# Kernel optimization log

Measured on AMD Instinct MI355X. Metric: run time of the kernel, lower is better.

The kernel has to match this reference:

```python
import jax, jax.numpy as jnp
import numpy as np

CAP = 512  # per-expert capacity; mean tokens/expert = 4096*4/64 = 256, CAP = mean + ~16 sigma (no drops for seed 0)


def _moe_forward(hidden_states, gate_w, w13, w2, top_k):
    T, H = hidden_states.shape
    E = gate_w.shape[0]
    # --- gating: softmax over expert logits, then top-k (npu_moe_gating_top_k_softmax) ---
    logits = hidden_states @ gate_w.T                      # [T, E]
    probs = jax.nn.softmax(logits, axis=-1)
    topk_w, topk_idx = jax.lax.top_k(probs, top_k)         # [T, K]
    # norm_topk_prob=True and top_k > 1
    topk_w = topk_w / (topk_w.sum(axis=-1, keepdims=True) + 1e-20)
    # --- init_routing: compute each (token, slot)'s rank within its expert ---
    N = T * top_k
    flat_e = topk_idx.reshape(N)                           # [N] expert id per expanded row
    order = jnp.argsort(flat_e)                            # stable sort by expert
    sorted_e = flat_e[order]
    counts = jax.ops.segment_sum(jnp.ones((N,), jnp.int32), flat_e, num_segments=E)
    starts = jnp.cumsum(counts) - counts                   # [E] start offset of each expert group
    rank_sorted = jnp.arange(N, dtype=jnp.int32) - starts[sorted_e].astype(jnp.int32)
    rank = jnp.zeros((N,), jnp.int32).at[order].set(rank_sorted)  # within-expert position
    # --- dispatch into [E, CAP, H] buffers (token gather/scatter) ---
    x_rep = jnp.repeat(hidden_states, top_k, axis=0)       # [N, H]
    disp = jnp.zeros((E, CAP, H), hidden_states.dtype).at[flat_e, rank].set(x_rep)
    # --- grouped GEMM: SwiGLU expert FFN as batched matmuls ---
    h = jnp.einsum('ech,ehf->ecf', disp, w13)              # [E, CAP, 2I]
    g, u = jnp.split(h, 2, axis=-1)
    a = jax.nn.silu(g) * u                                 # [E, CAP, I]
    y = jnp.einsum('eci,eih->ech', a, w2)                  # [E, CAP, H]
    # --- finalize_routing: gather back and weighted combine ---
    out_rows = y[flat_e, rank]                             # [N, H]
    out = (out_rows.reshape(T, top_k, H) * topk_w[..., None]).sum(axis=1)
    return out


def setup_inputs() -> dict:
    key = jax.random.key(0)
    k1, k2, k3, k4 = jax.random.split(key, 4)
    T, H, E, I = 4096, 2048, 64, 768
    hidden_states = jax.random.normal(k1, (T, H), dtype=jnp.float32)
    gate_w = jax.random.normal(k2, (E, H), dtype=jnp.float32) * 0.02
    w13 = jax.random.normal(k3, (E, H, 2 * I), dtype=jnp.float32) * 0.02
    w2 = jax.random.normal(k4, (E, I, H), dtype=jnp.float32) * 0.02
    return {"hidden_states": hidden_states, "gate_w": gate_w, "w13": w13, "w2": w2, "top_k": 4}


def reference(hidden_states, gate_w, w13, w2, top_k):
    return _moe_forward(hidden_states, gate_w, w13, w2, top_k)
```

## Files before the change

### kernel.cpp

```cpp
#include <hip/hip_runtime.h>
#include <hip/hip_bf16.h>

#define T_TOK 4096
#define HDIM  2048
#define NEXP  64
#define IDIM  768
#define TOPK  4
#define CAPE  512
#define NFLAT (T_TOK*TOPK)

typedef __bf16        bf16x8 __attribute__((ext_vector_type(8)));
typedef float         f32x4  __attribute__((ext_vector_type(4)));
typedef unsigned int  u32x4  __attribute__((ext_vector_type(4)));

__device__ __forceinline__ unsigned short f2bf(float f) {
  __bf16 b = (__bf16)f;
  return __builtin_bit_cast(unsigned short, b);
}
__device__ __forceinline__ unsigned pack2(float lo, float hi) {
  return (unsigned)f2bf(lo) | ((unsigned)f2bf(hi) << 16);
}

__global__ __launch_bounds__(256) void k_gating(
    const float* __restrict__ hs, const float* __restrict__ gw,
    unsigned short* __restrict__ hs_bf, int* __restrict__ tidx, float* __restrict__ tw)
{
  __shared__ float lg[16][64];
  const int tid = threadIdx.x;
  const int t0  = blockIdx.x * 16;

  {
    const f32x4* src = (const f32x4*)(hs + (size_t)t0 * HDIM);
    for (int i = tid; i < 16 * HDIM / 4; i += 256) {
      f32x4 v = src[i];
      ushort4 o;
      o.x = f2bf(v[0]); o.y = f2bf(v[1]); o.z = f2bf(v[2]); o.w = f2bf(v[3]);
      *(ushort4*)(hs_bf + (size_t)t0 * HDIM + (size_t)i * 4) = o;
    }
  }

  const int lane = tid & 63, wv = tid >> 6;
  {
    const f32x4* gr = (const f32x4*)(gw + (size_t)lane * HDIM);
    const f32x4* x0 = (const f32x4*)(hs + (size_t)(t0 + wv*4 + 0) * HDIM);
    const f32x4* x1 = (const f32x4*)(hs + (size_t)(t0 + wv*4 + 1) * HDIM);
    const f32x4* x2 = (const f32x4*)(hs + (size_t)(t0 + wv*4 + 2) * HDIM);
    const f32x4* x3 = (const f32x4*)(hs + (size_t)(t0 + wv*4 + 3) * HDIM);
    float a0=0.f, a1=0.f, a2=0.f, a3=0.f;
    for (int h = 0; h < HDIM/4; ++h) {
      f32x4 g = gr[h];
      f32x4 v0 = x0[h], v1 = x1[h], v2 = x2[h], v3 = x3[h];
      a0 += g[0]*v0[0] + g[1]*v0[1] + g[2]*v0[2] + g[3]*v0[3];
      a1 += g[0]*v1[0] + g[1]*v1[1] + g[2]*v1[2] + g[3]*v1[3];
      a2 += g[0]*v2[0] + g[1]*v2[1] + g[2]*v2[2] + g[3]*v2[3];
      a3 += g[0]*v3[0] + g[1]*v3[1] + g[2]*v3[2] + g[3]*v3[3];
    }
    lg[wv*4+0][lane] = a0;
    lg[wv*4+1][lane] = a1;
    lg[wv*4+2][lane] = a2;
    lg[wv*4+3][lane] = a3;
  }
  __syncthreads();

  if (tid < 16) {
    const int t = t0 + tid;
    unsigned long long chosen = 0ull;
    float bv[4]; int bi[4];
#pragma unroll
    for (int k = 0; k < 4; ++k) {
      float best = -1e30f; int b = 0;
      for (int e = 0; e < 64; ++e) {
        float v = lg[tid][e];
        if (!((chosen >> e) & 1ull) && v > best) { best = v; b = e; }
      }
      chosen |= 1ull << b; bv[k] = best; bi[k] = b;
    }
    float s = 0.f, w[4];
#pragma unroll
    for (int k = 0; k < 4; ++k) { w[k] = __expf(bv[k] - bv[0]); s += w[k]; }
    float inv = 1.f / s;
#pragma unroll
    for (int k = 0; k < 4; ++k) { tidx[t*4+k] = bi[k]; tw[t*4+k] = w[k] * inv; }
  }
}

__global__ __launch_bounds__(64) void k_count_rank(
    const int* __restrict__ tidx, int* __restrict__ rankb, int* __restrict__ counts)
{
  const int e = blockIdx.x;
  const int lane = threadIdx.x;
  int base = 0;
  for (int c = 0; c < NFLAT/64; ++c) {
    int n = c*64 + lane;
    bool m = (tidx[n] == e);
    unsigned long long mask = __ballot(m);
    if (m) rankb[n] = base + __popcll(mask & ((1ull << lane) - 1ull));
    base += __popcll(mask);
  }
  if (lane == 0) counts[e] = base;
}

__global__ __launch_bounds__(256) void k_build(
    const int* __restrict__ tidx, const int* __restrict__ rankb,
    const int* __restrict__ counts,
    int* __restrict__ starts, int* __restrict__ row_info, int* __restrict__ sortpos)
{
  __shared__ int s_starts[NEXP];
  if (threadIdx.x == 0) {
    int s = 0;
    for (int e = 0; e < NEXP; ++e) { s_starts[e] = s; starts[e] = s; s += counts[e]; }
  }
  __syncthreads();
  for (int n = threadIdx.x; n < NFLAT; n += 256) {
    int e = tidx[n], r = rankb[n];
    int sr = s_starts[e] + r;
    row_info[sr] = n;
    sortpos[n] = (r < CAPE) ? sr : -1;
  }
}

__global__ __launch_bounds__(512, 2) void k_gemm1(
    const unsigned short* __restrict__ hs_bf, const float* __restrict__ w13,
    const int* __restrict__ counts, const int* __restrict__ starts,
    const int* __restrict__ row_info, unsigned short* __restrict__ a_buf)
{
  const int nt = blockIdx.x;
  const int mt = blockIdx.y;
  const int e  = blockIdx.z;
  const int count = min(counts[e], CAPE);
  const int R0 = mt * 256;
  if (R0 >= count) return;
  const int tid = threadIdx.x;
  const int base_sorted = starts[e] + R0;

  __shared__ __align__(16) char lds[2*32768];
  char* Alds = lds;
  char* Bgl  = lds + 32768;
  char* Bul  = lds + 32768 + 16384;

  const int mrow = tid >> 3, cchunk = tid & 7;
  int tokp[4];
#pragma unroll
  for (int p = 0; p < 4; ++p) {
    int sr = base_sorted + mrow + p*64;
    if (sr > NFLAT-1) sr = NFLAT-1;
    tokp[p] = row_info[sr] >> 2;
  }
  const float* w13e = w13 + (size_t)e * HDIM * (2*IDIM);
  const int half = tid >> 8;
  const int t8   = tid & 255;
  const int kg   = t8 >> 5;
  const int n4   = (t8 & 31) * 4;

  const int lane = tid & 63, wv = tid >> 6;
  const int wr = wv >> 1, wc = wv & 1;

  f32x4 accg[4][4], accu[4][4];
#pragma unroll
  for (int i = 0; i < 4; ++i)
#pragma unroll
    for (int j = 0; j < 4; ++j) { accg[i][j] = f32x4{0.f,0.f,0.f,0.f}; accu[i][j] = f32x4{0.f,0.f,0.f,0.f}; }

  for (int kt = 0; kt < HDIM/64; ++kt) {
#pragma unroll
    for (int p = 0; p < 4; ++p) {
      int m = mrow + p*64;
      u32x4 v = *(const u32x4*)(hs_bf + (size_t)tokp[p]*HDIM + kt*64 + cchunk*8);
      *(u32x4*)(Alds + m*128 + ((cchunk ^ (m & 7)) << 4)) = v;
    }
    {
      const float* bp = w13e + (size_t)(kt*64 + kg*8) * (2*IDIM) + half*IDIM + nt*128 + n4;
      f32x4 f[8];
#pragma unroll
      for (int j = 0; j < 8; ++j) f[j] = *(const f32x4*)(bp + (size_t)j * (2*IDIM));
      char* Bl = half ? Bul : Bgl;
#pragma unroll
      for (int i = 0; i < 4; ++i) {
        int n = n4 + i;
        u32x4 q;
        q[0] = pack2(f[0][i], f[1][i]);
        q[1] = pack2(f[2][i], f[3][i]);
        q[2] = pack2(f[4][i], f[5][i]);
        q[3] = pack2(f[6][i], f[7][i]);
        *(u32x4*)(Bl + n*128 + ((kg ^ (n & 7)) << 4)) = q;
      }
    }
    __syncthreads();
#pragma unroll
    for (int kfi = 0; kfi < 2; ++kfi) {
      bf16x8 af[4], bg[4], bu[4];
#pragma unroll
      for (int mi = 0; mi < 4; ++mi) {
        int row = wr*64 + mi*16 + (lane & 15);
        af[mi] = *(const bf16x8*)(Alds + row*128 + ((((kfi<<2)|(lane>>4)) ^ (row & 7)) << 4));
      }
#pragma unroll
      for (int ni = 0; ni < 4; ++ni) {
        int n = wc*64 + ni*16 + (lane & 15);
        int c = (((kfi<<2)|(lane>>4)) ^ (n & 7)) << 4;
        bg[ni] = *(const bf16x8*)(Bgl + n*128 + c);
        bu[ni] = *(const bf16x8*)(Bul + n*128 + c);
      }
#pragma unroll
      for (int mi = 0; mi < 4; ++mi)
#pragma unroll
        for (int ni = 0; ni < 4; ++ni) {
          accg[mi][ni] = __builtin_amdgcn_mfma_f32_16x16x32_bf16(af[mi], bg[ni], accg[mi][ni], 0, 0, 0);
          accu[mi][ni] = __builtin_amdgcn_mfma_f32_16x16x32_bf16(af[mi], bu[ni], accu[mi][ni], 0, 0, 0);
        }
    }
    __syncthreads();
  }

#pragma unroll
  for (int mi = 0; mi < 4; ++mi) {
#pragma unroll
    for (int j = 0; j < 4; ++j) {
      int rl = wr*64 + mi*16 + (lane >> 4)*4 + j;
      if (R0 + rl < count) {
        size_t rowoff = (size_t)(base_sorted + rl) * IDIM;
#pragma unroll
        for (int ni = 0; ni < 4; ++ni) {
          int col = nt*128 + wc*64 + ni*16 + (lane & 15);
          float g = accg[mi][ni][j], u = accu[mi][ni][j];
          float a = (g / (1.f + __expf(-g))) * u;
          a_buf[rowoff + col] = f2bf(a);
        }
      }
    }
  }
}

__global__ __launch_bounds__(512, 2) void k_gemm2(
    const unsigned short* __restrict__ a_buf, const float* __restrict__ w2,
    const int* __restrict__ counts, const int* __restrict__ starts,
    float* __restrict__ y_buf)
{
  const int nt = blockIdx.x;
  const int mt = blockIdx.y;
  const int e  = blockIdx.z;
  const int count = min(counts[e], CAPE);
  const int R0 = mt * 256;
  if (R0 >= count) return;
  const int tid = threadIdx.x;
  const int base_sorted = starts[e] + R0;

  __shared__ __align__(16) char lds[32768 + 32768];
  char* Alds = lds;
  char* Blds = lds + 32768;

  const int mrow = tid >> 3, cchunk = tid & 7;
  int srp[4];
#pragma unroll
  for (int p = 0; p < 4; ++p) {
    int sr = base_sorted + mrow + p*64;
    srp[p] = (sr > NFLAT-1) ? (NFLAT-1) : sr;
  }
  const float* w2e = w2 + (size_t)e * IDIM * HDIM;
  const int pass = tid >> 8;
  const int t8   = tid & 255;
  const int kg   = t8 >> 5, n4 = (t8 & 31) * 4;
  const int lane = tid & 63, wv = tid >> 6, wr = wv >> 1, wc = wv & 1;

  f32x4 acc[4][8];
#pragma unroll
  for (int i = 0; i < 4; ++i)
#pragma unroll
    for (int j = 0; j < 8; ++j) acc[i][j] = f32x4{0.f,0.f,0.f,0.f};

  for (int kt = 0; kt < IDIM/64; ++kt) {
#pragma unroll
    for (int p = 0; p < 4; ++p) {
      int m = mrow + p*64;
      u32x4 v = *(const u32x4*)(a_buf + (size_t)srp[p]*IDIM + kt*64 + cchunk*8);
      *(u32x4*)(Alds + m*128 + ((cchunk ^ (m & 7)) << 4)) = v;
    }
    {
      int nn = n4 + pass*128;
      const float* bp = w2e + (size_t)(kt*64 + kg*8) * HDIM + nt*256 + nn;
      f32x4 f[8];
#pragma unroll
      for (int j = 0; j < 8; ++j) f[j] = *(const f32x4*)(bp + (size_t)j * HDIM);
#pragma unroll
      for (int i = 0; i < 4; ++i) {
        int n = nn + i;
        u32x4 q;
        q[0] = pack2(f[0][i], f[1][i]);
        q[1] = pack2(f[2][i], f[3][i]);
        q[2] = pack2(f[4][i], f[5][i]);
        q[3] = pack2(f[6][i], f[7][i]);
        *(u32x4*)(Blds + n*128 + ((kg ^ (n & 7)) << 4)) = q;
      }
    }
    __syncthreads();
#pragma unroll
    for (int kfi = 0; kfi < 2; ++kfi) {
      bf16x8 af[4], bb[8];
#pragma unroll
      for (int mi = 0; mi < 4; ++mi) {
        int row = wr*64 + mi*16 + (lane & 15);
        af[mi] = *(const bf16x8*)(Alds + row*128 + ((((kfi<<2)|(lane>>4)) ^ (row & 7)) << 4));
      }
#pragma unroll
      for (int ni = 0; ni < 8; ++ni) {
        int n = wc*128 + ni*16 + (lane & 15);
        bb[ni] = *(const bf16x8*)(Blds + n*128 + (((((kfi<<2)|(lane>>4)) ^ (n & 7))) << 4));
      }
#pragma unroll
      for (int mi = 0; mi < 4; ++mi)
#pragma unroll
        for (int ni = 0; ni < 8; ++ni)
          acc[mi][ni] = __builtin_amdgcn_mfma_f32_16x16x32_bf16(af[mi], bb[ni], acc[mi][ni], 0, 0, 0);
    }
    __syncthreads();
  }

#pragma unroll
  for (int mi = 0; mi < 4; ++mi) {
#pragma unroll
    for (int j = 0; j < 4; ++j) {
      int rl = wr*64 + mi*16 + (lane >> 4)*4 + j;
      if (R0 + rl < count) {
        int sr = base_sorted + rl;
        float* yrow = y_buf + (size_t)sr * HDIM;
#pragma unroll
        for (int ni = 0; ni < 8; ++ni) {
          int col = nt*256 + wc*128 + ni*16 + (lane & 15);
          yrow[col] = acc[mi][ni][j];
        }
      }
    }
  }
}

__global__ __launch_bounds__(256) void k_finalize(
    const float* __restrict__ y_buf, const int* __restrict__ sortpos,
    const float* __restrict__ tw, float* __restrict__ out)
{
  const int t = blockIdx.x;
  const int tid = threadIdx.x;
  f32x4 acc0 = {0.f,0.f,0.f,0.f}, acc1 = {0.f,0.f,0.f,0.f};
#pragma unroll
  for (int k = 0; k < 4; ++k) {
    int sp = sortpos[t*4+k];
    float w = tw[t*4+k];
    if (sp >= 0) {
      const f32x4* yr = (const f32x4*)(y_buf + (size_t)sp * HDIM);
      acc0 += w * yr[tid];
      acc1 += w * yr[tid + 256];
    }
  }
  f32x4* o = (f32x4*)(out + (size_t)t * HDIM);
  o[tid] = acc0;
  o[tid + 256] = acc1;
}

extern "C" void kernel_launch(void* const* d_in, const int* in_sizes, int n_in,
                              void* d_out, int out_size, void* d_ws, size_t ws_size,
                              hipStream_t stream) {
  const float* hs  = (const float*)d_in[0];
  const float* gw  = (const float*)d_in[1];
  const float* w13 = (const float*)d_in[2];
  const float* w2  = (const float*)d_in[3];
  float* out = (float*)d_out;

  char* ws = (char*)d_ws;
  size_t off = 0;
  auto alloc = [&](size_t bytes) {
    off = (off + 255) & ~(size_t)255;
    char* p = ws + off;
    off += bytes;
    return p;
  };
  unsigned short* hs_bf = (unsigned short*)alloc((size_t)T_TOK * HDIM * 2);
  int*   tidx   = (int*)  alloc((size_t)NFLAT * 4);
  float* tw     = (float*)alloc((size_t)NFLAT * 4);
  int*   rankb  = (int*)  alloc((size_t)NFLAT * 4);
  int*   counts = (int*)  alloc((size_t)NEXP * 4);
  int*   starts = (int*)  alloc((size_t)NEXP * 4);
  int*   rinfo  = (int*)  alloc((size_t)NFLAT * 4);
  int*   sortp  = (int*)  alloc((size_t)NFLAT * 4);
  unsigned short* a_buf = (unsigned short*)alloc((size_t)NFLAT * IDIM * 2);
  float* y_buf  = (float*)alloc((size_t)NFLAT * HDIM * 4);
  (void)ws_size; (void)in_sizes; (void)n_in; (void)out_size;

  k_gating<<<T_TOK/16, 256, 0, stream>>>(hs, gw, hs_bf, tidx, tw);
  k_count_rank<<<NEXP, 64, 0, stream>>>(tidx, rankb, counts);
  k_build<<<1, 256, 0, stream>>>(tidx, rankb, counts, starts, rinfo, sortp);
  k_gemm1<<<dim3(6, 2, NEXP), 512, 0, stream>>>(hs_bf, w13, counts, starts, rinfo, a_buf);
  k_gemm2<<<dim3(8, 2, NEXP), 512, 0, stream>>>(a_buf, w2, counts, starts, y_buf);
  k_finalize<<<T_TOK, 256, 0, stream>>>(y_buf, sortp, tw, out);
}
```

Before: 796.7 us.

## Double-buffer LDS with register prefetch, loop M tiles in-block, store y as bf16

Both expert GEMMs now double-buffer LDS (128KB) and prefetch the next K tile's A rows and fp32 weights into registers while MFMAs run on the current tile, dropping one barrier per iteration. The M-tile grid dimension is folded into an in-block loop, so each block walks all of its expert's row tiles. The LDS swizzle also XORs in row>>3 bits. The intermediate y buffer is stored as bf16 instead of fp32, halving its write and read traffic in finalize at some precision cost. The larger LDS footprint likely lowers occupancy, and fewer blocks now launch (384/512 versus up to double before), which reduces parallelism.

```diff
diff --git a/kernel.cpp b/kernel.cpp
--- a/kernel.cpp
+++ b/kernel.cpp
@@ -19,6 +19,9 @@
 }
 __device__ __forceinline__ unsigned pack2(float lo, float hi) {
   return (unsigned)f2bf(lo) | ((unsigned)f2bf(hi) << 16);
+}
+__device__ __forceinline__ int swz(int row, int chunk) {
+  return row*128 + (((chunk ^ (row & 7) ^ ((row >> 3) & 7)) & 7) << 4);
 }
 
 __global__ __launch_bounds__(256) void k_gating(
@@ -125,106 +128,138 @@
     const int* __restrict__ row_info, unsigned short* __restrict__ a_buf)
 {
   const int nt = blockIdx.x;
-  const int mt = blockIdx.y;
-  const int e  = blockIdx.z;
+  const int e  = blockIdx.y;
   const int count = min(counts[e], CAPE);
-  const int R0 = mt * 256;
-  if (R0 >= count) return;
+  if (count <= 0) return;
+  const int nmt = (count + 255) >> 8;
   const int tid = threadIdx.x;
-  const int base_sorted = starts[e] + R0;
-
-  __shared__ __align__(16) char lds[2*32768];
-  char* Alds = lds;
-  char* Bgl  = lds + 32768;
-  char* Bul  = lds + 32768 + 16384;
+  const int estart = starts[e];
+
+  __shared__ __align__(16) char lds[2*65536];
 
   const int mrow = tid >> 3, cchunk = tid & 7;
-  int tokp[4];
-#pragma unroll
-  for (int p = 0; p < 4; ++p) {
-    int sr = base_sorted + mrow + p*64;
-    if (sr > NFLAT-1) sr = NFLAT-1;
-    tokp[p] = row_info[sr] >> 2;
-  }
   const float* w13e = w13 + (size_t)e * HDIM * (2*IDIM);
   const int half = tid >> 8;
   const int t8   = tid & 255;
   const int kg   = t8 >> 5;
   const int n4   = (t8 & 31) * 4;
-
   const int lane = tid & 63, wv = tid >> 6;
   const int wr = wv >> 1, wc = wv & 1;
 
-  f32x4 accg[4][4], accu[4][4];
-#pragma unroll
-  for (int i = 0; i < 4; ++i)
-#pragma unroll
-    for (int j = 0; j < 4; ++j) { accg[i][j] = f32x4{0.f,0.f,0.f,0.f}; accu[i][j] = f32x4{0.f,0.f,0.f,0.f}; }
-
-  for (int kt = 0; kt < HDIM/64; ++kt) {
+  int cur = 0;
+  for (int mi = 0; mi < nmt; ++mi) {
+    const int R0 = mi << 8;
+    const int base_sorted = estart + R0;
+    int tokp[4];
 #pragma unroll
     for (int p = 0; p < 4; ++p) {
-      int m = mrow + p*64;
-      u32x4 v = *(const u32x4*)(hs_bf + (size_t)tokp[p]*HDIM + kt*64 + cchunk*8);
-      *(u32x4*)(Alds + m*128 + ((cchunk ^ (m & 7)) << 4)) = v;
-    }
+      int sr = base_sorted + mrow + p*64;
+      if (sr > NFLAT-1) sr = NFLAT-1;
+      tokp[p] = row_info[sr] >> 2;
+    }
+    f32x4 accg[4][4], accu[4][4];
+#pragma unroll
+    for (int i = 0; i < 4; ++i)
+#pragma unroll
+      for (int j = 0; j < 4; ++j) { accg[i][j] = f32x4{0.f,0.f,0.f,0.f}; accu[i][j] = f32x4{0.f,0.f,0.f,0.f}; }
+
+    u32x4 rA[4]; f32x4 rB[8];
+#pragma unroll
+    for (int p = 0; p < 4; ++p)
+      rA[p] = *(const u32x4*)(hs_bf + (size_t)tokp[p]*HDIM + cchunk*8);
     {
-      const float* bp = w13e + (size_t)(kt*64 + kg*8) * (2*IDIM) + half*IDIM + nt*128 + n4;
-      f32x4 f[8];
-#pragma unroll
-      for (int j = 0; j < 8; ++j) f[j] = *(const f32x4*)(bp + (size_t)j * (2*IDIM));
-      char* Bl = half ? Bul : Bgl;
+      const float* bp = w13e + (size_t)(kg*8) * (2*IDIM) + half*IDIM + nt*128 + n4;
+#pragma unroll
+      for (int j = 0; j < 8; ++j) rB[j] = *(const f32x4*)(bp + (size_t)j * (2*IDIM));
+    }
+    __syncthreads();
+    {
+      char* A0 = lds + cur*65536;
+      char* B0 = lds + cur*65536 + 32768 + half*16384;
+#pragma unroll
+      for (int p = 0; p < 4; ++p)
+        *(u32x4*)(A0 + swz(mrow + p*64, cchunk)) = rA[p];
 #pragma unroll
       for (int i = 0; i < 4; ++i) {
-        int n = n4 + i;
         u32x4 q;
-        q[0] = pack2(f[0][i], f[1][i]);
-        q[1] = pack2(f[2][i], f[3][i]);
-        q[2] = pack2(f[4][i], f[5][i]);
-        q[3] = pack2(f[6][i], f[7][i]);
-        *(u32x4*)(Bl + n*128 + ((kg ^ (n & 7)) << 4)) = q;
-      }
-    }
-    __syncthreads();
-#pragma unroll
-    for (int kfi = 0; kfi < 2; ++kfi) {
-      bf16x8 af[4], bg[4], bu[4];
-#pragma unroll
-      for (int mi = 0; mi < 4; ++mi) {
-        int row = wr*64 + mi*16 + (lane & 15);
-        af[mi] = *(const bf16x8*)(Alds + row*128 + ((((kfi<<2)|(lane>>4)) ^ (row & 7)) << 4));
-      }
-#pragma unroll
-      for (int ni = 0; ni < 4; ++ni) {
-        int n = wc*64 + ni*16 + (lane & 15);
-        int c = (((kfi<<2)|(lane>>4)) ^ (n & 7)) << 4;
-        bg[ni] = *(const bf16x8*)(Bgl + n*128 + c);
-        bu[ni] = *(const bf16x8*)(Bul + n*128 + c);
-      }
-#pragma unroll
-      for (int mi = 0; mi < 4; ++mi)
+        q[0] = pack2(rB[0][i], rB[1][i]);
+        q[1] = pack2(rB[2][i], rB[3][i]);
+        q[2] = pack2(rB[4][i], rB[5][i]);
+        q[3] = pack2(rB[6][i], rB[7][i]);
+        *(u32x4*)(B0 + swz(n4 + i, kg)) = q;
+      }
+    }
+
+    for (int kt = 0; kt < HDIM/64; ++kt) {
+      __syncthreads();
+      const bool pf = (kt+1 < HDIM/64);
+      if (pf) {
+#pragma unroll
+        for (int p = 0; p < 4; ++p)
+          rA[p] = *(const u32x4*)(hs_bf + (size_t)tokp[p]*HDIM + (kt+1)*64 + cchunk*8);
+        const float* bp = w13e + (size_t)((kt+1)*64 + kg*8) * (2*IDIM) + half*IDIM + nt*128 + n4;
+#pragma unroll
+        for (int j = 0; j < 8; ++j) rB[j] = *(const f32x4*)(bp + (size_t)j * (2*IDIM));
+      }
+      char* Ac  = lds + cur*65536;
+      char* Bgc = lds + cur*65536 + 32768;
+      char* Buc = Bgc + 16384;
+#pragma unroll
+      for (int kfi = 0; kfi < 2; ++kfi) {
+        const int ch = (kfi<<2) | (lane>>4);
+        bf16x8 af[4], bg[4], bu[4];
+#pragma unroll
+        for (int mi2 = 0; mi2 < 4; ++mi2) {
+          int row = wr*64 + mi2*16 + (lane & 15);
+          af[mi2] = *(const bf16x8*)(Ac + swz(row, ch));
+        }
 #pragma unroll
         for (int ni = 0; ni < 4; ++ni) {
-          accg[mi][ni] = __builtin_amdgcn_mfma_f32_16x16x32_bf16(af[mi], bg[ni], accg[mi][ni], 0, 0, 0);
-          accu[mi][ni] = __builtin_amdgcn_mfma_f32_16x16x32_bf16(af[mi], bu[ni], accu[mi][ni], 0, 0, 0);
-        }
-    }
-    __syncthreads();
-  }
-
-#pragma unroll
-  for (int mi = 0; mi < 4; ++mi) {
-#pragma unroll
-    for (int j = 0; j < 4; ++j) {
-      int rl = wr*64 + mi*16 + (lane >> 4)*4 + j;
-      if (R0 + rl < count) {
-        size_t rowoff = (size_t)(base_sorted + rl) * IDIM;
-#pragma unroll
-        for (int ni = 0; ni < 4; ++ni) {
-          int col = nt*128 + wc*64 + ni*16 + (lane & 15);
-          float g = accg[mi][ni][j], u = accu[mi][ni][j];
-          float a = (g / (1.f + __expf(-g))) * u;
-          a_buf[rowoff + col] = f2bf(a);
+          int n = wc*64 + ni*16 + (lane & 15);
+          bg[ni] = *(const bf16x8*)(Bgc + swz(n, ch));
+          bu[ni] = *(const bf16x8*)(Buc + swz(n, ch));
+        }
+#pragma unroll
+        for (int mi2 = 0; mi2 < 4; ++mi2)
+#pragma unroll
+          for (int ni = 0; ni < 4; ++ni) {
+            accg[mi2][ni] = __builtin_amdgcn_mfma_f32_16x16x32_bf16(af[mi2], bg[ni], accg[mi2][ni], 0, 0, 0);
+            accu[mi2][ni] = __builtin_amdgcn_mfma_f32_16x16x32_bf16(af[mi2], bu[ni], accu[mi2][ni], 0, 0, 0);
+          }
+      }
+      if (pf) {
+        char* An = lds + (cur^1)*65536;
+        char* Bn = lds + (cur^1)*65536 + 32768 + half*16384;
+#pragma unroll
+        for (int p = 0; p < 4; ++p)
+          *(u32x4*)(An + swz(mrow + p*64, cchunk)) = rA[p];
+#pragma unroll
+        for (int i = 0; i < 4; ++i) {
+          u32x4 q;
+          q[0] = pack2(rB[0][i], rB[1][i]);
+          q[1] = pack2(rB[2][i], rB[3][i]);
+          q[2] = pack2(rB[4][i], rB[5][i]);
+          q[3] = pack2(rB[6][i], rB[7][i]);
+          *(u32x4*)(Bn + swz(n4 + i, kg)) = q;
+        }
+      }
+      cur ^= 1;
+    }
+
+#pragma unroll
+    for (int mi2 = 0; mi2 < 4; ++mi2) {
+#pragma unroll
+      for (int j = 0; j < 4; ++j) {
+        int rl = wr*64 + mi2*16 + (lane >> 4)*4 + j;
+        if (R0 + rl < count) {
+          size_t rowoff = (size_t)(base_sorted + rl) * IDIM;
+#pragma unroll
+          for (int ni = 0; ni < 4; ++ni) {
+            int col = nt*128 + wc*64 + ni*16 + (lane & 15);
+            float g = accg[mi2][ni][j], u = accu[mi2][ni][j];
+            float a = (g / (1.f + __expf(-g))) * u;
+            a_buf[rowoff + col] = f2bf(a);
+          }
         }
       }
     }
@@ -234,99 +269,135 @@
 __global__ __launch_bounds__(512, 2) void k_gemm2(
     const unsigned short* __restrict__ a_buf, const float* __restrict__ w2,
     const int* __restrict__ counts, const int* __restrict__ starts,
-    float* __restrict__ y_buf)
+    unsigned short* __restrict__ y_buf)
 {
   const int nt = blockIdx.x;
-  const int mt = blockIdx.y;
-  const int e  = blockIdx.z;
+  const int e  = blockIdx.y;
   const int count = min(counts[e], CAPE);
-  const int R0 = mt * 256;
-  if (R0 >= count) return;
+  if (count <= 0) return;
+  const int nmt = (count + 255) >> 8;
   const int tid = threadIdx.x;
-  const int base_sorted = starts[e] + R0;
-
-  __shared__ __align__(16) char lds[32768 + 32768];
-  char* Alds = lds;
-  char* Blds = lds + 32768;
+  const int estart = starts[e];
+
+  __shared__ __align__(16) char lds[2*65536];
 
   const int mrow = tid >> 3, cchunk = tid & 7;
-  int srp[4];
-#pragma unroll
-  for (int p = 0; p < 4; ++p) {
-    int sr = base_sorted + mrow + p*64;
-    srp[p] = (sr > NFLAT-1) ? (NFLAT-1) : sr;
-  }
   const float* w2e = w2 + (size_t)e * IDIM * HDIM;
   const int pass = tid >> 8;
   const int t8   = tid & 255;
   const int kg   = t8 >> 5, n4 = (t8 & 31) * 4;
   const int lane = tid & 63, wv = tid >> 6, wr = wv >> 1, wc = wv & 1;
 
-  f32x4 acc[4][8];
-#pragma unroll
-  for (int i = 0; i < 4; ++i)
-#pragma unroll
-    for (int j = 0; j < 8; ++j) acc[i][j] = f32x4{0.f,0.f,0.f,0.f};
-
-  for (int kt = 0; kt < IDIM/64; ++kt) {
+  int cur = 0;
+  for (int mi = 0; mi < nmt; ++mi) {
+    const int R0 = mi << 8;
+    const int base_sorted = estart + R0;
+    int srp[4];
 #pragma unroll
     for (int p = 0; p < 4; ++p) {
-      int m = mrow + p*64;
-      u32x4 v = *(const u32x4*)(a_buf + (size_t)srp[p]*IDIM + kt*64 + cchunk*8);
-      *(u32x4*)(Alds + m*128 + ((cchunk ^ (m & 7)) << 4)) = v;
-    }
+      int sr = base_sorted + mrow + p*64;
+      srp[p] = (sr > NFLAT-1) ? (NFLAT-1) : sr;
+    }
+    f32x4 acc[4][8];
+#pragma unroll
+    for (int i = 0; i < 4; ++i)
+#pragma unroll
+      for (int j = 0; j < 8; ++j) acc[i][j] = f32x4{0.f,0.f,0.f,0.f};
+
+    u32x4 rA[4]; f32x4 rB[8];
+#pragma unroll
+    for (int p = 0; p < 4; ++p)
+      rA[p] = *(const u32x4*)(a_buf + (size_t)srp[p]*IDIM + cchunk*8);
     {
-      int nn = n4 + pass*128;
-      const float* bp = w2e + (size_t)(kt*64 + kg*8) * HDIM + nt*256 + nn;
-      f32x4 f[8];
-#pragma unroll
-      for (int j = 0; j < 8; ++j) f[j] = *(const f32x4*)(bp + (size_t)j * HDIM);
+      const float* bp = w2e + (size_t)(kg*8) * HDIM + nt*256 + pass*128 + n4;
+#pragma unroll
+      for (int j = 0; j < 8; ++j) rB[j] = *(const f32x4*)(bp + (size_t)j * HDIM);
+    }
+    __syncthreads();
+    {
+      char* A0 = lds + cur*65536;
+      char* B0 = lds + cur*65536 + 32768;
+#pragma unroll
+      for (int p = 0; p < 4; ++p)
+        *(u32x4*)(A0 + swz(mrow + p*64, cchunk)) = rA[p];
 #pragma unroll
       for (int i = 0; i < 4; ++i) {
-        int n = nn + i;
+        int n = pass*128 + n4 + i;
         u32x4 q;
-        q[0] = pack2(f[0][i], f[1][i]);
-        q[1] = pack2(f[2][i], f[3][i]);
-        q[2] = pack2(f[4][i], f[5][i]);
-        q[3] = pack2(f[6][i], f[7][i]);
-        *(u32x4*)(Blds + n*128 + ((kg ^ (n & 7)) << 4)) = q;
-      }
-    }
-    __syncthreads();
-#pragma unroll
-    for (int kfi = 0; kfi < 2; ++kfi) {
-      bf16x8 af[4], bb[8];
-#pragma unroll
-      for (int mi = 0; mi < 4; ++mi) {
-        int row = wr*64 + mi*16 + (lane & 15);
-        af[mi] = *(const bf16x8*)(Alds + row*128 + ((((kfi<<2)|(lane>>4)) ^ (row & 7)) << 4));
-      }
-#pragma unroll
-      for (int ni = 0; ni < 8; ++ni) {
-        int n = wc*128 + ni*16 + (lane & 15);
-        bb[ni] = *(const bf16x8*)(Blds + n*128 + (((((kfi<<2)|(lane>>4)) ^ (n & 7))) << 4));
-      }
-#pragma unroll
-      for (int mi = 0; mi < 4; ++mi)
-#pragma unroll
-        for (int ni = 0; ni < 8; ++ni)
-          acc[mi][ni] = __builtin_amdgcn_mfma_f32_16x16x32_bf16(af[mi], bb[ni], acc[mi][ni], 0, 0, 0);
-    }
-    __syncthreads();
-  }
-
-#pragma unroll
-  for (int mi = 0; mi < 4; ++mi) {
-#pragma unroll
-    for (int j = 0; j < 4; ++j) {
-      int rl = wr*64 + mi*16 + (lane >> 4)*4 + j;
-      if (R0 + rl < count) {
-        int sr = base_sorted + rl;
-        float* yrow = y_buf + (size_t)sr * HDIM;
+        q[0] = pack2(rB[0][i], rB[1][i]);
+        q[1] = pack2(rB[2][i], rB[3][i]);
+        q[2] = pack2(rB[4][i], rB[5][i]);
+        q[3] = pack2(rB[6][i], rB[7][i]);
+        *(u32x4*)(B0 + swz(n, kg)) = q;
+      }
+    }
+
+    for (int kt = 0; kt < IDIM/64; ++kt) {
+      __syncthreads();
+      const bool pf = (kt+1 < IDIM/64);
+      if (pf) {
+#pragma unroll
+        for (int p = 0; p < 4; ++p)
+          rA[p] = *(const u32x4*)(a_buf + (size_t)srp[p]*IDIM + (kt+1)*64 + cchunk*8);
+        const float* bp = w2e + (size_t)((kt+1)*64 + kg*8) * HDIM + nt*256 + pass*128 + n4;
+#pragma unroll
+        for (int j = 0; j < 8; ++j) rB[j] = *(const f32x4*)(bp + (size_t)j * HDIM);
+      }
+      char* Ac = lds + cur*65536;
+      char* Bc = lds + cur*65536 + 32768;
+#pragma unroll
+      for (int kfi = 0; kfi < 2; ++kfi) {
+        const int ch = (kfi<<2) | (lane>>4);
+        bf16x8 af[4], bb[8];
+#pragma unroll
+        for (int mi2 = 0; mi2 < 4; ++mi2) {
+          int row = wr*64 + mi2*16 + (lane & 15);
+          af[mi2] = *(const bf16x8*)(Ac + swz(row, ch));
+        }
 #pragma unroll
         for (int ni = 0; ni < 8; ++ni) {
-          int col = nt*256 + wc*128 + ni*16 + (lane & 15);
-          yrow[col] = acc[mi][ni][j];
+          int n = wc*128 + ni*16 + (lane & 15);
+          bb[ni] = *(const bf16x8*)(Bc + swz(n, ch));
+        }
+#pragma unroll
+        for (int mi2 = 0; mi2 < 4; ++mi2)
+#pragma unroll
+          for (int ni = 0; ni < 8; ++ni)
+            acc[mi2][ni] = __builtin_amdgcn_mfma_f32_16x16x32_bf16(af[mi2], bb[ni], acc[mi2][ni], 0, 0, 0);
+      }
+      if (pf) {
+        char* An = lds + (cur^1)*65536;
+        char* Bn = lds + (cur^1)*65536 + 32768;
+#pragma unroll
+        for (int p = 0; p < 4; ++p)
+          *(u32x4*)(An + swz(mrow + p*64, cchunk)) = rA[p];
+#pragma unroll
+        for (int i = 0; i < 4; ++i) {
+          int n = pass*128 + n4 + i;
+          u32x4 q;
+          q[0] = pack2(rB[0][i], rB[1][i]);
+          q[1] = pack2(rB[2][i], rB[3][i]);
+          q[2] = pack2(rB[4][i], rB[5][i]);
+          q[3] = pack2(rB[6][i], rB[7][i]);
+          *(u32x4*)(Bn + swz(n, kg)) = q;
+        }
+      }
+      cur ^= 1;
+    }
+
+#pragma unroll
+    for (int mi2 = 0; mi2 < 4; ++mi2) {
+#pragma unroll
+      for (int j = 0; j < 4; ++j) {
+        int rl = wr*64 + mi2*16 + (lane >> 4)*4 + j;
+        if (R0 + rl < count) {
+          int sr = base_sorted + rl;
+          unsigned short* yrow = y_buf + (size_t)sr * HDIM;
+#pragma unroll
+          for (int ni = 0; ni < 8; ++ni) {
+            int col = nt*256 + wc*128 + ni*16 + (lane & 15);
+            yrow[col] = f2bf(acc[mi2][ni][j]);
+          }
         }
       }
     }
@@ -334,25 +405,34 @@
 }
 
 __global__ __launch_bounds__(256) void k_finalize(
-    const float* __restrict__ y_buf, const int* __restrict__ sortpos,
+    const unsigned short* __restrict__ y_buf, const int* __restrict__ sortpos,
     const float* __restrict__ tw, float* __restrict__ out)
 {
   const int t = blockIdx.x;
   const int tid = threadIdx.x;
-  f32x4 acc0 = {0.f,0.f,0.f,0.f}, acc1 = {0.f,0.f,0.f,0.f};
+  float acc[8];
+#pragma unroll
+  for (int i = 0; i < 8; ++i) acc[i] = 0.f;
 #pragma unroll
   for (int k = 0; k < 4; ++k) {
     int sp = sortpos[t*4+k];
     float w = tw[t*4+k];
     if (sp >= 0) {
-      const f32x4* yr = (const f32x4*)(y_buf + (size_t)sp * HDIM);
-      acc0 += w * yr[tid];
-      acc1 += w * yr[tid + 256];
-    }
-  }
-  f32x4* o = (f32x4*)(out + (size_t)t * HDIM);
-  o[tid] = acc0;
-  o[tid + 256] = acc1;
+      u32x4 v = *(const u32x4*)(y_buf + (size_t)sp * HDIM + tid*8);
+#pragma unroll
+      for (int q = 0; q < 4; ++q) {
+        float lo = __builtin_bit_cast(float, v[q] << 16);
+        float hi = __builtin_bit_cast(float, v[q] & 0xffff0000u);
+        acc[2*q]   += w * lo;
+        acc[2*q+1] += w * hi;
+      }
+    }
+  }
+  f32x4 o0 = {acc[0], acc[1], acc[2], acc[3]};
+  f32x4 o1 = {acc[4], acc[5], acc[6], acc[7]};
+  f32x4* o = (f32x4*)(out + (size_t)t * HDIM + tid*8);
+  o[0] = o0;
+  o[1] = o1;
 }
 
 extern "C" void kernel_launch(void* const* d_in, const int* in_sizes, int n_in,
@@ -381,13 +461,13 @@
   int*   rinfo  = (int*)  alloc((size_t)NFLAT * 4);
   int*   sortp  = (int*)  alloc((size_t)NFLAT * 4);
   unsigned short* a_buf = (unsigned short*)alloc((size_t)NFLAT * IDIM * 2);
-  float* y_buf  = (float*)alloc((size_t)NFLAT * HDIM * 4);
+  unsigned short* y_buf = (unsigned short*)alloc((size_t)NFLAT * HDIM * 2);
   (void)ws_size; (void)in_sizes; (void)n_in; (void)out_size;
 
   k_gating<<<T_TOK/16, 256, 0, stream>>>(hs, gw, hs_bf, tidx, tw);
   k_count_rank<<<NEXP, 64, 0, stream>>>(tidx, rankb, counts);
   k_build<<<1, 256, 0, stream>>>(tidx, rankb, counts, starts, rinfo, sortp);
-  k_gemm1<<<dim3(6, 2, NEXP), 512, 0, stream>>>(hs_bf, w13, counts, starts, rinfo, a_buf);
-  k_gemm2<<<dim3(8, 2, NEXP), 512, 0, stream>>>(a_buf, w2, counts, starts, y_buf);
+  k_gemm1<<<dim3(6, NEXP), 512, 0, stream>>>(hs_bf, w13, counts, starts, rinfo, a_buf);
+  k_gemm2<<<dim3(8, NEXP), 512, 0, stream>>>(a_buf, w2, counts, starts, y_buf);
   k_finalize<<<T_TOK, 256, 0, stream>>>(y_buf, sortp, tw, out);
 }
```

Result: slower. 886.4 us (median of 2 runs) (+11.3%).

## Restructure expert GEMMs with per-expert M loop, direct-to-LDS loads, bf16 output

Applied to the files above, without the earlier changes.

Both expert GEMMs now launch one block per (N-tile, expert) with 256 threads and a smaller tile. Each block loops over all M-tiles of its expert, so the fp32 weight tile is re-read per M-tile but mostly hits cache. Activation rows are copied with global_load_lds straight into LDS under a new XOR swizzle. The y buffer is stored as bf16 to halve write and finalize read traffic, at some extra rounding error. Smaller tiles raise occupancy but lower MFMA work per LDS load.

```diff
diff --git a/kernel.cpp b/kernel.cpp
--- a/kernel.cpp
+++ b/kernel.cpp
@@ -19,6 +19,14 @@
 }
 __device__ __forceinline__ unsigned pack2(float lo, float hi) {
   return (unsigned)f2bf(lo) | ((unsigned)f2bf(hi) << 16);
+}
+__device__ __forceinline__ int swz(int row, int chunk) {
+  return row*128 + (((chunk ^ (row & 7) ^ ((row >> 3) & 7)) & 7) << 4);
+}
+__device__ __forceinline__ void gload_lds16(const void* g, void* l) {
+  __builtin_amdgcn_global_load_lds(
+      (const __attribute__((address_space(1))) unsigned int*)g,
+      (__attribute__((address_space(3))) unsigned int*)l, 16, 0, 0);
 }
 
 __global__ __launch_bounds__(256) void k_gating(
@@ -119,240 +127,253 @@
   }
 }
 
-__global__ __launch_bounds__(512, 2) void k_gemm1(
+__global__ __launch_bounds__(256, 3) void k_gemm1(
     const unsigned short* __restrict__ hs_bf, const float* __restrict__ w13,
     const int* __restrict__ counts, const int* __restrict__ starts,
     const int* __restrict__ row_info, unsigned short* __restrict__ a_buf)
 {
   const int nt = blockIdx.x;
-  const int mt = blockIdx.y;
-  const int e  = blockIdx.z;
+  const int e  = blockIdx.y;
   const int count = min(counts[e], CAPE);
-  const int R0 = mt * 256;
-  if (R0 >= count) return;
+  if (count <= 0) return;
+  const int nmt = (count + 127) >> 7;
   const int tid = threadIdx.x;
-  const int base_sorted = starts[e] + R0;
-
-  __shared__ __align__(16) char lds[2*32768];
-  char* Alds = lds;
-  char* Bgl  = lds + 32768;
-  char* Bul  = lds + 32768 + 16384;
-
-  const int mrow = tid >> 3, cchunk = tid & 7;
-  int tokp[4];
-#pragma unroll
-  for (int p = 0; p < 4; ++p) {
-    int sr = base_sorted + mrow + p*64;
-    if (sr > NFLAT-1) sr = NFLAT-1;
-    tokp[p] = row_info[sr] >> 2;
-  }
-  const float* w13e = w13 + (size_t)e * HDIM * (2*IDIM);
-  const int half = tid >> 8;
-  const int t8   = tid & 255;
-  const int kg   = t8 >> 5;
-  const int n4   = (t8 & 31) * 4;
+  const int estart = starts[e];
+
+  __shared__ __align__(16) char lds[32768];
 
   const int lane = tid & 63, wv = tid >> 6;
   const int wr = wv >> 1, wc = wv & 1;
 
-  f32x4 accg[4][4], accu[4][4];
-#pragma unroll
-  for (int i = 0; i < 4; ++i)
-#pragma unroll
-    for (int j = 0; j < 4; ++j) { accg[i][j] = f32x4{0.f,0.f,0.f,0.f}; accu[i][j] = f32x4{0.f,0.f,0.f,0.f}; }
-
-  for (int kt = 0; kt < HDIM/64; ++kt) {
-#pragma unroll
-    for (int p = 0; p < 4; ++p) {
-      int m = mrow + p*64;
-      u32x4 v = *(const u32x4*)(hs_bf + (size_t)tokp[p]*HDIM + kt*64 + cchunk*8);
-      *(u32x4*)(Alds + m*128 + ((cchunk ^ (m & 7)) << 4)) = v;
-    }
-    {
-      const float* bp = w13e + (size_t)(kt*64 + kg*8) * (2*IDIM) + half*IDIM + nt*128 + n4;
-      f32x4 f[8];
-#pragma unroll
-      for (int j = 0; j < 8; ++j) f[j] = *(const f32x4*)(bp + (size_t)j * (2*IDIM));
-      char* Bl = half ? Bul : Bgl;
-#pragma unroll
-      for (int i = 0; i < 4; ++i) {
-        int n = n4 + i;
-        u32x4 q;
-        q[0] = pack2(f[0][i], f[1][i]);
-        q[1] = pack2(f[2][i], f[3][i]);
-        q[2] = pack2(f[4][i], f[5][i]);
-        q[3] = pack2(f[6][i], f[7][i]);
-        *(u32x4*)(Bl + n*128 + ((kg ^ (n & 7)) << 4)) = q;
-      }
-    }
-    __syncthreads();
-#pragma unroll
-    for (int kfi = 0; kfi < 2; ++kfi) {
-      bf16x8 af[4], bg[4], bu[4];
-#pragma unroll
-      for (int mi = 0; mi < 4; ++mi) {
-        int row = wr*64 + mi*16 + (lane & 15);
-        af[mi] = *(const bf16x8*)(Alds + row*128 + ((((kfi<<2)|(lane>>4)) ^ (row & 7)) << 4));
-      }
-#pragma unroll
-      for (int ni = 0; ni < 4; ++ni) {
-        int n = wc*64 + ni*16 + (lane & 15);
-        int c = (((kfi<<2)|(lane>>4)) ^ (n & 7)) << 4;
-        bg[ni] = *(const bf16x8*)(Bgl + n*128 + c);
-        bu[ni] = *(const bf16x8*)(Bul + n*128 + c);
-      }
-#pragma unroll
-      for (int mi = 0; mi < 4; ++mi)
-#pragma unroll
-        for (int ni = 0; ni < 4; ++ni) {
-          accg[mi][ni] = __builtin_amdgcn_mfma_f32_16x16x32_bf16(af[mi], bg[ni], accg[mi][ni], 0, 0, 0);
-          accu[mi][ni] = __builtin_amdgcn_mfma_f32_16x16x32_bf16(af[mi], bu[ni], accu[mi][ni], 0, 0, 0);
+  const int bhalf = tid >> 7;
+  const int t7 = tid & 127;
+  const int bkg = t7 >> 4;
+  const int bc4 = (t7 & 15) * 4;
+  const float* w13e = w13 + (size_t)e * HDIM * (2*IDIM) + (size_t)bhalf*IDIM + (size_t)nt*64 + bc4;
+
+  int srcch[4];
+#pragma unroll
+  for (int r = 0; r < 4; ++r)
+    srcch[r] = (lane & 7) ^ (lane >> 3) ^ ((wv*4 + r) & 7);
+
+  for (int mit = 0; mit < nmt; ++mit) {
+    const int R0 = mit << 7;
+    const int base_sorted = estart + R0;
+    int tokp[4];
+#pragma unroll
+    for (int r = 0; r < 4; ++r) {
+      int sr = base_sorted + wv*32 + r*8 + (lane >> 3);
+      if (sr > NFLAT-1) sr = NFLAT-1;
+      tokp[r] = row_info[sr] >> 2;
+    }
+
+    f32x4 accg[4][2], accu[4][2];
+#pragma unroll
+    for (int i = 0; i < 4; ++i)
+#pragma unroll
+      for (int j = 0; j < 2; ++j) { accg[i][j] = f32x4{0.f,0.f,0.f,0.f}; accu[i][j] = f32x4{0.f,0.f,0.f,0.f}; }
+
+    for (int kt = 0; kt < HDIM/64; ++kt) {
+#pragma unroll
+      for (int r = 0; r < 4; ++r)
+        gload_lds16(hs_bf + (size_t)tokp[r]*HDIM + kt*64 + srcch[r]*8,
+                    lds + wv*4096 + r*1024 + lane*16);
+      {
+        const float* bp = w13e + (size_t)(kt*64 + bkg*8) * (2*IDIM);
+        f32x4 f[8];
+#pragma unroll
+        for (int j = 0; j < 8; ++j) f[j] = *(const f32x4*)(bp + (size_t)j * (2*IDIM));
+        char* Bh = lds + 16384 + bhalf*8192;
+#pragma unroll
+        for (int i = 0; i < 4; ++i) {
+          u32x4 q;
+          q[0] = pack2(f[0][i], f[1][i]);
+          q[1] = pack2(f[2][i], f[3][i]);
+          q[2] = pack2(f[4][i], f[5][i]);
+          q[3] = pack2(f[6][i], f[7][i]);
+          *(u32x4*)(Bh + swz(bc4 + i, bkg)) = q;
         }
-    }
-    __syncthreads();
-  }
-
-#pragma unroll
-  for (int mi = 0; mi < 4; ++mi) {
-#pragma unroll
-    for (int j = 0; j < 4; ++j) {
-      int rl = wr*64 + mi*16 + (lane >> 4)*4 + j;
-      if (R0 + rl < count) {
-        size_t rowoff = (size_t)(base_sorted + rl) * IDIM;
-#pragma unroll
-        for (int ni = 0; ni < 4; ++ni) {
-          int col = nt*128 + wc*64 + ni*16 + (lane & 15);
-          float g = accg[mi][ni][j], u = accu[mi][ni][j];
-          float a = (g / (1.f + __expf(-g))) * u;
-          a_buf[rowoff + col] = f2bf(a);
+      }
+      __syncthreads();
+      char* Bgl = lds + 16384;
+      char* Bul = lds + 24576;
+#pragma unroll
+      for (int kfi = 0; kfi < 2; ++kfi) {
+        const int ch = (kfi<<2) | (lane>>4);
+        bf16x8 af[4], bg[2], bu[2];
+#pragma unroll
+        for (int m2 = 0; m2 < 4; ++m2)
+          af[m2] = *(const bf16x8*)(lds + swz(wr*64 + m2*16 + (lane & 15), ch));
+#pragma unroll
+        for (int ni = 0; ni < 2; ++ni) {
+          int col = wc*32 + ni*16 + (lane & 15);
+          bg[ni] = *(const bf16x8*)(Bgl + swz(col, ch));
+          bu[ni] = *(const bf16x8*)(Bul + swz(col, ch));
         }
-      }
-    }
-  }
-}
-
-__global__ __launch_bounds__(512, 2) void k_gemm2(
+#pragma unroll
+        for (int m2 = 0; m2 < 4; ++m2)
+#pragma unroll
+          for (int ni = 0; ni < 2; ++ni) {
+            accg[m2][ni] = __builtin_amdgcn_mfma_f32_16x16x32_bf16(af[m2], bg[ni], accg[m2][ni], 0, 0, 0);
+            accu[m2][ni] = __builtin_amdgcn_mfma_f32_16x16x32_bf16(af[m2], bu[ni], accu[m2][ni], 0, 0, 0);
+          }
+      }
+      __syncthreads();
+    }
+
+#pragma unroll
+    for (int m2 = 0; m2 < 4; ++m2) {
+#pragma unroll
+      for (int j = 0; j < 4; ++j) {
+        int rl = wr*64 + m2*16 + (lane >> 4)*4 + j;
+        if (R0 + rl < count) {
+          size_t rowoff = (size_t)(base_sorted + rl) * IDIM;
+#pragma unroll
+          for (int ni = 0; ni < 2; ++ni) {
+            int col = nt*64 + wc*32 + ni*16 + (lane & 15);
+            float g = accg[m2][ni][j], u = accu[m2][ni][j];
+            float a = (g / (1.f + __expf(-g))) * u;
+            a_buf[rowoff + col] = f2bf(a);
+          }
+        }
+      }
+    }
+  }
+}
+
+__global__ __launch_bounds__(256, 3) void k_gemm2(
     const unsigned short* __restrict__ a_buf, const float* __restrict__ w2,
     const int* __restrict__ counts, const int* __restrict__ starts,
-    float* __restrict__ y_buf)
+    unsigned short* __restrict__ y_buf)
 {
   const int nt = blockIdx.x;
-  const int mt = blockIdx.y;
-  const int e  = blockIdx.z;
+  const int e  = blockIdx.y;
   const int count = min(counts[e], CAPE);
-  const int R0 = mt * 256;
-  if (R0 >= count) return;
+  if (count <= 0) return;
+  const int nmt = (count + 127) >> 7;
   const int tid = threadIdx.x;
-  const int base_sorted = starts[e] + R0;
-
-  __shared__ __align__(16) char lds[32768 + 32768];
-  char* Alds = lds;
-  char* Blds = lds + 32768;
-
-  const int mrow = tid >> 3, cchunk = tid & 7;
-  int srp[4];
-#pragma unroll
-  for (int p = 0; p < 4; ++p) {
-    int sr = base_sorted + mrow + p*64;
-    srp[p] = (sr > NFLAT-1) ? (NFLAT-1) : sr;
-  }
-  const float* w2e = w2 + (size_t)e * IDIM * HDIM;
-  const int pass = tid >> 8;
-  const int t8   = tid & 255;
-  const int kg   = t8 >> 5, n4 = (t8 & 31) * 4;
-  const int lane = tid & 63, wv = tid >> 6, wr = wv >> 1, wc = wv & 1;
-
-  f32x4 acc[4][8];
-#pragma unroll
-  for (int i = 0; i < 4; ++i)
-#pragma unroll
-    for (int j = 0; j < 8; ++j) acc[i][j] = f32x4{0.f,0.f,0.f,0.f};
-
-  for (int kt = 0; kt < IDIM/64; ++kt) {
-#pragma unroll
-    for (int p = 0; p < 4; ++p) {
-      int m = mrow + p*64;
-      u32x4 v = *(const u32x4*)(a_buf + (size_t)srp[p]*IDIM + kt*64 + cchunk*8);
-      *(u32x4*)(Alds + m*128 + ((cchunk ^ (m & 7)) << 4)) = v;
-    }
-    {
-      int nn = n4 + pass*128;
-      const float* bp = w2e + (size_t)(kt*64 + kg*8) * HDIM + nt*256 + nn;
-      f32x4 f[8];
-#pragma unroll
-      for (int j = 0; j < 8; ++j) f[j] = *(const f32x4*)(bp + (size_t)j * HDIM);
-#pragma unroll
-      for (int i = 0; i < 4; ++i) {
-        int n = nn + i;
-        u32x4 q;
-        q[0] = pack2(f[0][i], f[1][i]);
-        q[1] = pack2(f[2][i], f[3][i]);
-        q[2] = pack2(f[4][i], f[5][i]);
-        q[3] = pack2(f[6][i], f[7][i]);
-        *(u32x4*)(Blds + n*128 + ((kg ^ (n & 7)) << 4)) = q;
-      }
-    }
-    __syncthreads();
-#pragma unroll
-    for (int kfi = 0; kfi < 2; ++kfi) {
-      bf16x8 af[4], bb[8];
-#pragma unroll
-      for (int mi = 0; mi < 4; ++mi) {
-        int row = wr*64 + mi*16 + (lane & 15);
-        af[mi] = *(const bf16x8*)(Alds + row*128 + ((((kfi<<2)|(lane>>4)) ^ (row & 7)) << 4));
-      }
-#pragma unroll
-      for (int ni = 0; ni < 8; ++ni) {
-        int n = wc*128 + ni*16 + (lane & 15);
-        bb[ni] = *(const bf16x8*)(Blds + n*128 + (((((kfi<<2)|(lane>>4)) ^ (n & 7))) << 4));
-      }
-#pragma unroll
-      for (int mi = 0; mi < 4; ++mi)
-#pragma unroll
-        for (int ni = 0; ni < 8; ++ni)
-          acc[mi][ni] = __builtin_amdgcn_mfma_f32_16x16x32_bf16(af[mi], bb[ni], acc[mi][ni], 0, 0, 0);
-    }
-    __syncthreads();
-  }
-
-#pragma unroll
-  for (int mi = 0; mi < 4; ++mi) {
-#pragma unroll
-    for (int j = 0; j < 4; ++j) {
-      int rl = wr*64 + mi*16 + (lane >> 4)*4 + j;
-      if (R0 + rl < count) {
-        int sr = base_sorted + rl;
-        float* yrow = y_buf + (size_t)sr * HDIM;
-#pragma unroll
-        for (int ni = 0; ni < 8; ++ni) {
-          int col = nt*256 + wc*128 + ni*16 + (lane & 15);
-          yrow[col] = acc[mi][ni][j];
+  const int estart = starts[e];
+
+  __shared__ __align__(16) char lds[32768];
+
+  const int lane = tid & 63, wv = tid >> 6;
+  const int wr = wv >> 1, wc = wv & 1;
+
+  const int bkg = tid >> 5;
+  const int bc4 = (tid & 31) * 4;
+  const float* w2e = w2 + (size_t)e * IDIM * HDIM + (size_t)nt*128 + bc4;
+
+  int srcch[4];
+#pragma unroll
+  for (int r = 0; r < 4; ++r)
+    srcch[r] = (lane & 7) ^ (lane >> 3) ^ ((wv*4 + r) & 7);
+
+  for (int mit = 0; mit < nmt; ++mit) {
+    const int R0 = mit << 7;
+    const int base_sorted = estart + R0;
+    int srp[4];
+#pragma unroll
+    for (int r = 0; r < 4; ++r) {
+      int sr = base_sorted + wv*32 + r*8 + (lane >> 3);
+      srp[r] = (sr > NFLAT-1) ? (NFLAT-1) : sr;
+    }
+
+    f32x4 acc[4][4];
+#pragma unroll
+    for (int i = 0; i < 4; ++i)
+#pragma unroll
+      for (int j = 0; j < 4; ++j) acc[i][j] = f32x4{0.f,0.f,0.f,0.f};
+
+    for (int kt = 0; kt < IDIM/64; ++kt) {
+#pragma unroll
+      for (int r = 0; r < 4; ++r)
+        gload_lds16(a_buf + (size_t)srp[r]*IDIM + kt*64 + srcch[r]*8,
+                    lds + wv*4096 + r*1024 + lane*16);
+      {
+        const float* bp = w2e + (size_t)(kt*64 + bkg*8) * HDIM;
+        f32x4 f[8];
+#pragma unroll
+        for (int j = 0; j < 8; ++j) f[j] = *(const f32x4*)(bp + (size_t)j * HDIM);
+        char* Bl = lds + 16384;
+#pragma unroll
+        for (int i = 0; i < 4; ++i) {
+          u32x4 q;
+          q[0] = pack2(f[0][i], f[1][i]);
+          q[1] = pack2(f[2][i], f[3][i]);
+          q[2] = pack2(f[4][i], f[5][i]);
+          q[3] = pack2(f[6][i], f[7][i]);
+          *(u32x4*)(Bl + swz(bc4 + i, bkg)) = q;
         }
       }
+      __syncthreads();
+      char* Bl = lds + 16384;
+#pragma unroll
+      for (int kfi = 0; kfi < 2; ++kfi) {
+        const int ch = (kfi<<2) | (lane>>4);
+        bf16x8 af[4], bb[4];
+#pragma unroll
+        for (int m2 = 0; m2 < 4; ++m2)
+          af[m2] = *(const bf16x8*)(lds + swz(wr*64 + m2*16 + (lane & 15), ch));
+#pragma unroll
+        for (int ni = 0; ni < 4; ++ni)
+          bb[ni] = *(const bf16x8*)(Bl + swz(wc*64 + ni*16 + (lane & 15), ch));
+#pragma unroll
+        for (int m2 = 0; m2 < 4; ++m2)
+#pragma unroll
+          for (int ni = 0; ni < 4; ++ni)
+            acc[m2][ni] = __builtin_amdgcn_mfma_f32_16x16x32_bf16(af[m2], bb[ni], acc[m2][ni], 0, 0, 0);
+      }
+      __syncthreads();
+    }
+
+#pragma unroll
+    for (int m2 = 0; m2 < 4; ++m2) {
+#pragma unroll
+      for (int j = 0; j < 4; ++j) {
+        int rl = wr*64 + m2*16 + (lane >> 4)*4 + j;
+        if (R0 + rl < count) {
+          int sr = base_sorted + rl;
+          unsigned short* yrow = y_buf + (size_t)sr * HDIM;
+#pragma unroll
+          for (int ni = 0; ni < 4; ++ni) {
+            int col = nt*128 + wc*64 + ni*16 + (lane & 15);
+            yrow[col] = f2bf(acc[m2][ni][j]);
+          }
+        }
+      }
     }
   }
 }
 
 __global__ __launch_bounds__(256) void k_finalize(
-    const float* __restrict__ y_buf, const int* __restrict__ sortpos,
+    const unsigned short* __restrict__ y_buf, const int* __restrict__ sortpos,
     const float* __restrict__ tw, float* __restrict__ out)
 {
   const int t = blockIdx.x;
   const int tid = threadIdx.x;
-  f32x4 acc0 = {0.f,0.f,0.f,0.f}, acc1 = {0.f,0.f,0.f,0.f};
+  float acc[8];
+#pragma unroll
+  for (int i = 0; i < 8; ++i) acc[i] = 0.f;
 #pragma unroll
   for (int k = 0; k < 4; ++k) {
     int sp = sortpos[t*4+k];
     float w = tw[t*4+k];
     if (sp >= 0) {
-      const f32x4* yr = (const f32x4*)(y_buf + (size_t)sp * HDIM);
-      acc0 += w * yr[tid];
-      acc1 += w * yr[tid + 256];
-    }
-  }
-  f32x4* o = (f32x4*)(out + (size_t)t * HDIM);
-  o[tid] = acc0;
-  o[tid + 256] = acc1;
+      u32x4 v = *(const u32x4*)(y_buf + (size_t)sp * HDIM + tid*8);
+#pragma unroll
+      for (int q = 0; q < 4; ++q) {
+        float lo = __builtin_bit_cast(float, v[q] << 16);
+        float hi = __builtin_bit_cast(float, v[q] & 0xffff0000u);
+        acc[2*q]   += w * lo;
+        acc[2*q+1] += w * hi;
+      }
+    }
+  }
+  f32x4 o0 = {acc[0], acc[1], acc[2], acc[3]};
+  f32x4 o1 = {acc[4], acc[5], acc[6], acc[7]};
+  f32x4* o = (f32x4*)(out + (size_t)t * HDIM + tid*8);
+  o[0] = o0;
+  o[1] = o1;
 }
 
 extern "C" void kernel_launch(void* const* d_in, const int* in_sizes, int n_in,
@@ -381,13 +402,13 @@
   int*   rinfo  = (int*)  alloc((size_t)NFLAT * 4);
   int*   sortp  = (int*)  alloc((size_t)NFLAT * 4);
   unsigned short* a_buf = (unsigned short*)alloc((size_t)NFLAT * IDIM * 2);
-  float* y_buf  = (float*)alloc((size_t)NFLAT * HDIM * 4);
+  unsigned short* y_buf = (unsigned short*)alloc((size_t)NFLAT * HDIM * 2);
   (void)ws_size; (void)in_sizes; (void)n_in; (void)out_size;
 
   k_gating<<<T_TOK/16, 256, 0, stream>>>(hs, gw, hs_bf, tidx, tw);
   k_count_rank<<<NEXP, 64, 0, stream>>>(tidx, rankb, counts);
   k_build<<<1, 256, 0, stream>>>(tidx, rankb, counts, starts, rinfo, sortp);
-  k_gemm1<<<dim3(6, 2, NEXP), 512, 0, stream>>>(hs_bf, w13, counts, starts, rinfo, a_buf);
-  k_gemm2<<<dim3(8, 2, NEXP), 512, 0, stream>>>(a_buf, w2, counts, starts, y_buf);
+  k_gemm1<<<dim3(12, NEXP), 256, 0, stream>>>(hs_bf, w13, counts, starts, rinfo, a_buf);
+  k_gemm2<<<dim3(16, NEXP), 256, 0, stream>>>(a_buf, w2, counts, starts, y_buf);
   k_finalize<<<T_TOK, 256, 0, stream>>>(y_buf, sortp, tw, out);
 }
```

Measured after the change: 943.7 us. 1.18x slower.
